# Kernel tuning notes

Measured on AMD Instinct MI355X. Metric: run time of the kernel, lower is better.

Reference implementation:

```python
import jax, jax.numpy as jnp
import numpy as np

M = 8192          # tokens (batch*seq)
K = 4096          # in_features
N = 4096          # out_features
BK = 64           # block_k (row_block of B)
BN = 64           # block_n (col_block of B)
NR = K // BK      # 64 block rows of B
NC = N // BN      # 64 block cols of B
OCC = 4           # nonzero blocks per column (and per row)
TB = NR * OCC     # total nonzero blocks = 256


def _build_indices():
    # Regular block mask: each column has OCC nonzero block-rows, each row has OCC
    # nonzero block-cols (matches BlockMask.regular invariants). Deterministic
    # construction: column c uses rows (c + s*(NR//OCC)) % NR, sorted ascending.
    step = NR // OCC
    cols = np.arange(NC)
    rows = np.sort((cols[None, :] + step * np.arange(OCC)[:, None]) % NR, axis=0)  # [OCC, NC]
    # _build_data_indices assigns data slots column-major, row-ascending within a
    # column, so column c's blocks (sorted by row) get slots c*OCC + s.
    data = cols[None, :] * OCC + np.arange(OCC)[:, None]  # [OCC, NC]
    return rows.astype(np.int32), data.astype(np.int32)


def setup_inputs() -> dict:
    key = jax.random.key(0)
    k1, k2 = jax.random.split(key)
    rows, data = _build_indices()
    return {
        "A": jax.random.normal(k1, (M, K), dtype=jnp.float32),
        "B_data": jax.random.normal(k2, (BK, BN * TB), dtype=jnp.float32) * 0.02,
        "row_indices": jnp.asarray(rows),
        "data_indices": jnp.asarray(data),
    }


def reference(A, B_data, row_indices, data_indices):
    # A: [M, K]; B_data: [BK, BN*TB]; indices: [OCC, NC]
    m, k = A.shape
    occ, nc = row_indices.shape
    bk = B_data.shape[0]
    tb = occ * nc
    bn = B_data.shape[1] // tb
    nr = k // bk
    # Gather A blocks per (sub_k, out_col): [m, occ, nc, bk]
    A_blocks = A.reshape(m, nr, bk)[:, row_indices]
    # Gather B blocks: B_data laid out as [bk, tb, bn] -> [tb, bk, bn] -> [occ, nc, bk, bn]
    B_blocks = jnp.transpose(B_data.reshape(bk, tb, bn), (1, 0, 2))[data_indices]
    # Accumulate over occ and bk (fp32 accumulation like the Triton kernel)
    C = jnp.einsum('mock,ockn->mcn', A_blocks, B_blocks,
                   preferred_element_type=jnp.float32)
    return C.reshape(m, nc * bn).astype(A.dtype)
```

## Files before the change

kernel.cpp:

```cpp
#include <hip/hip_runtime.h>
#include <hip/hip_bf16.h>

typedef __bf16 bf16x8 __attribute__((ext_vector_type(8)));
typedef float  f32x4  __attribute__((ext_vector_type(4)));

__device__ __forceinline__ void dma16(const float* g, float* l) {
    typedef const __attribute__((address_space(1))) unsigned int* gp_t;
    typedef __attribute__((address_space(3))) unsigned int*       lp_t;
    __builtin_amdgcn_global_load_lds((gp_t)(const void*)g, (lp_t)(void*)l, 16, 0, 0);
}

__global__ __launch_bounds__(256, 2) void sparse_linear_kernel(
    const float* __restrict__ A, const float* __restrict__ Bd,
    const int* __restrict__ rowi, const int* __restrict__ di,
    float* __restrict__ C)
{
    __shared__ __align__(16) float Aring[4][3][16 * 64];
    __shared__ __align__(16) unsigned short Bt[4 * 64 * 64];
    char* BtB = (char*)Bt;

    const int bid = blockIdx.x;
    const int c   = bid & 63;
    const int grp = bid >> 6;
    const int t    = threadIdx.x;
    const int lane = t & 63;
    const int w    = t >> 6;

    int rs[4], ds[4];
    #pragma unroll
    for (int s = 0; s < 4; ++s) {
        rs[s] = rowi[s * 64 + c];
        ds[s] = di[s * 64 + c];
    }
    int koff[4];
    #pragma unroll
    for (int s = 0; s < 4; ++s) koff[s] = rs[s] * 64;

    const long wrow0 = (long)grp * 1024 + w * 64;

    auto dmaA = [&](int q, int kb, int mt, int slot) {
        float* slotp = &Aring[w][slot][0];
        #pragma unroll
        for (int i = 0; i < 4; ++i) {
            const int rr  = i * 4 + (lane >> 4);
            const int kfl = (((lane & 15) * 16) ^ (rr << 4)) >> 2;
            const float* g = A + (wrow0 + q * 256 + mt * 16 + rr) * 4096 + koff[kb] + kfl;
            dma16(g, slotp + i * 256);
        }
    };

    dmaA(0, 0, 0, 0);
    dmaA(0, 0, 1, 1);
    dmaA(0, 0, 2, 2);

    {
        const int n  = t & 63;
        const int sb = t >> 6;
        const float* Bg = Bd + (long)ds[sb] * 64 + n;
        char* dst = BtB + sb * 8192 + n * 128;
        const int sw = (n & 7) << 4;
        #pragma unroll
        for (int k4 = 0; k4 < 16; ++k4) {
            union { ushort4 u4; __bf16 e[4]; } pk;
            pk.e[0] = (__bf16)Bg[(long)(4 * k4 + 0) * 16384];
            pk.e[1] = (__bf16)Bg[(long)(4 * k4 + 1) * 16384];
            pk.e[2] = (__bf16)Bg[(long)(4 * k4 + 2) * 16384];
            pk.e[3] = (__bf16)Bg[(long)(4 * k4 + 3) * 16384];
            *(ushort4*)(dst + ((8 * k4) ^ sw)) = pk.u4;
        }
    }
    __syncthreads();

    f32x4 acc[4][4];
    #pragma unroll
    for (int m = 0; m < 4; ++m)
        #pragma unroll
        for (int n2 = 0; n2 < 4; ++n2) acc[m][n2] = f32x4{0.f, 0.f, 0.f, 0.f};

    bf16x8 bfr[2][4];

    #pragma unroll 1
    for (int q = 0; q < 4; ++q) {
        const int qm3 = q % 3;

        #pragma unroll
        for (int local = 0; local < 16; ++local) {
            const int kb = local >> 2, mt = local & 3;
            int slot = qm3 + (local % 3);
            if (slot >= 3) slot -= 3;

            if (local < 3) asm volatile("s_waitcnt vmcnt(24)" ::: "memory");
            else           asm volatile("s_waitcnt vmcnt(8)"  ::: "memory");
            __builtin_amdgcn_sched_barrier(0);

            if (mt == 0) {
                const char* bbase = BtB + kb * 8192;
                #pragma unroll
                for (int kh = 0; kh < 2; ++kh)
                    #pragma unroll
                    for (int n2 = 0; n2 < 4; ++n2) {
                        const int nr = n2 * 16 + (lane & 15);
                        const int kbyte = kh * 64 + (lane >> 4) * 16;
                        bfr[kh][n2] = *(const bf16x8*)(bbase + nr * 128 + (kbyte ^ ((nr & 7) << 4)));
                    }
            }

            const char* ab = (const char*)&Aring[w][slot][0];
            const int r   = lane & 15;
            const int q32 = (lane >> 4) * 32;
            f32x4 a0 = *(const f32x4*)(ab + r * 256 + ((q32)            ^ (r << 4)));
            f32x4 a1 = *(const f32x4*)(ab + r * 256 + ((q32 + 16)       ^ (r << 4)));
            f32x4 a2 = *(const f32x4*)(ab + r * 256 + ((128 + q32)      ^ (r << 4)));
            f32x4 a3 = *(const f32x4*)(ab + r * 256 + ((128 + q32 + 16) ^ (r << 4)));
            union { bf16x8 v; __bf16 e[8]; } af0, af1;
            #pragma unroll
            for (int i = 0; i < 4; ++i) {
                af0.e[i]     = (__bf16)a0[i];
                af0.e[i + 4] = (__bf16)a1[i];
                af1.e[i]     = (__bf16)a2[i];
                af1.e[i + 4] = (__bf16)a3[i];
            }

            __builtin_amdgcn_s_setprio(1);
            #pragma unroll
            for (int kh = 0; kh < 2; ++kh) {
                const bf16x8 afv = kh ? af1.v : af0.v;
                #pragma unroll
                for (int n2 = 0; n2 < 4; ++n2)
                    acc[mt][n2] = __builtin_amdgcn_mfma_f32_16x16x32_bf16(afv, bfr[kh][n2], acc[mt][n2], 0, 0, 0);
            }
            __builtin_amdgcn_s_setprio(0);

            {
                int l2 = local + 3, q2 = q;
                if (l2 >= 16) { l2 -= 16; ++q2; }
                if (q2 > 3) q2 = 3;
                dmaA(q2, l2 >> 2, l2 & 3, slot);
            }

            if (local == 15) {
                __builtin_amdgcn_sched_barrier(0);
                #pragma unroll
                for (int mts = 0; mts < 4; ++mts) {
                    const long crow0 = wrow0 + q * 256 + mts * 16 + (lane >> 4) * 4;
                    const long col0  = (long)c * 64 + (lane & 15);
                    #pragma unroll
                    for (int n2 = 0; n2 < 4; ++n2) {
                        #pragma unroll
                        for (int v = 0; v < 4; ++v)
                            __builtin_nontemporal_store(acc[mts][n2][v],
                                &C[(crow0 + v) * 4096 + col0 + n2 * 16]);
                        acc[mts][n2] = f32x4{0.f, 0.f, 0.f, 0.f};
                    }
                }
                __builtin_amdgcn_sched_barrier(0);
            }
        }
    }

    asm volatile("s_waitcnt vmcnt(0)" ::: "memory");
}

extern "C" void kernel_launch(void* const* d_in, const int* in_sizes, int n_in,
                              void* d_out, int out_size, void* d_ws, size_t ws_size,
                              hipStream_t stream) {
    const float* A    = (const float*)d_in[0];
    const float* Bd   = (const float*)d_in[1];
    const int*   rowi = (const int*)d_in[2];
    const int*   di   = (const int*)d_in[3];
    float*       C    = (float*)d_out;

    dim3 grid(8 * 64);
    dim3 block(256);
    hipLaunchKernelGGL(sparse_linear_kernel, grid, block, 0, stream,
                       A, Bd, rowi, di, C);
}
```

Measured before the change: 56.25 us.

## Use 512-thread blocks with a 4-deep A ring and interleaved output stores

```diff
diff --git a/kernel.cpp b/kernel.cpp
--- a/kernel.cpp
+++ b/kernel.cpp
@@ -10,12 +10,12 @@
     __builtin_amdgcn_global_load_lds((gp_t)(const void*)g, (lp_t)(void*)l, 16, 0, 0);
 }
 
-__global__ __launch_bounds__(256, 2) void sparse_linear_kernel(
+__global__ __launch_bounds__(512, 2) void sparse_linear_kernel(
     const float* __restrict__ A, const float* __restrict__ Bd,
     const int* __restrict__ rowi, const int* __restrict__ di,
     float* __restrict__ C)
 {
-    __shared__ __align__(16) float Aring[4][3][16 * 64];
+    __shared__ __align__(16) float Aring[8][4][1024];
     __shared__ __align__(16) unsigned short Bt[4 * 64 * 64];
     char* BtB = (char*)Bt;
 
@@ -26,25 +26,23 @@
     const int lane = t & 63;
     const int w    = t >> 6;
 
-    int rs[4], ds[4];
+    int ds[4], koff[4];
     #pragma unroll
     for (int s = 0; s < 4; ++s) {
-        rs[s] = rowi[s * 64 + c];
-        ds[s] = di[s * 64 + c];
+        koff[s] = rowi[s * 64 + c] * 64;
+        ds[s]   = di[s * 64 + c];
     }
-    int koff[4];
-    #pragma unroll
-    for (int s = 0; s < 4; ++s) koff[s] = rs[s] * 64;
 
-    const long wrow0 = (long)grp * 1024 + w * 64;
+    const long wrow0 = (long)grp * 2048 + w * 256;
 
     auto dmaA = [&](int q, int kb, int mt, int slot) {
         float* slotp = &Aring[w][slot][0];
+        const long rbase = wrow0 + q * 64 + mt * 16;
         #pragma unroll
         for (int i = 0; i < 4; ++i) {
             const int rr  = i * 4 + (lane >> 4);
             const int kfl = (((lane & 15) * 16) ^ (rr << 4)) >> 2;
-            const float* g = A + (wrow0 + q * 256 + mt * 16 + rr) * 4096 + koff[kb] + kfl;
+            const float* g = A + (rbase + rr) * 4096 + koff[kb] + kfl;
             dma16(g, slotp + i * 256);
         }
     };
@@ -52,21 +50,23 @@
     dmaA(0, 0, 0, 0);
     dmaA(0, 0, 1, 1);
     dmaA(0, 0, 2, 2);
+    dmaA(0, 0, 3, 3);
 
     {
         const int n  = t & 63;
-        const int sb = t >> 6;
-        const float* Bg = Bd + (long)ds[sb] * 64 + n;
+        const int kh = (t >> 6) & 1;
+        const int sb = t >> 7;
+        const float* Bg = Bd + (long)ds[sb] * 64 + (long)kh * 32 * 16384 + n;
         char* dst = BtB + sb * 8192 + n * 128;
         const int sw = (n & 7) << 4;
         #pragma unroll
-        for (int k4 = 0; k4 < 16; ++k4) {
+        for (int k4 = 0; k4 < 8; ++k4) {
             union { ushort4 u4; __bf16 e[4]; } pk;
             pk.e[0] = (__bf16)Bg[(long)(4 * k4 + 0) * 16384];
             pk.e[1] = (__bf16)Bg[(long)(4 * k4 + 1) * 16384];
             pk.e[2] = (__bf16)Bg[(long)(4 * k4 + 2) * 16384];
             pk.e[3] = (__bf16)Bg[(long)(4 * k4 + 3) * 16384];
-            *(ushort4*)(dst + ((8 * k4) ^ sw)) = pk.u4;
+            *(ushort4*)(dst + ((kh * 64 + 8 * k4) ^ sw)) = pk.u4;
         }
     }
     __syncthreads();
@@ -79,19 +79,39 @@
 
     bf16x8 bfr[2][4];
 
-    #pragma unroll 1
+    #pragma unroll
     for (int q = 0; q < 4; ++q) {
-        const int qm3 = q % 3;
-
         #pragma unroll
         for (int local = 0; local < 16; ++local) {
+            const int st = q * 16 + local;
             const int kb = local >> 2, mt = local & 3;
-            int slot = qm3 + (local % 3);
-            if (slot >= 3) slot -= 3;
+            const int slot = st & 3;
 
-            if (local < 3) asm volatile("s_waitcnt vmcnt(24)" ::: "memory");
-            else           asm volatile("s_waitcnt vmcnt(8)"  ::: "memory");
-            __builtin_amdgcn_sched_barrier(0);
+            if (q == 3 && local == 13)      asm volatile("s_waitcnt vmcnt(8)"  ::: "memory");
+            else if (q == 3 && local == 14) asm volatile("s_waitcnt vmcnt(4)"  ::: "memory");
+            else if (q == 3 && local == 15) asm volatile("s_waitcnt vmcnt(0)"  ::: "memory");
+            else if (q >= 1 && (local == 1 || local == 6))
+                                            asm volatile("s_waitcnt vmcnt(28)" ::: "memory");
+            else if (q >= 1 && (local == 2 || local == 5))
+                                            asm volatile("s_waitcnt vmcnt(44)" ::: "memory");
+            else if (q >= 1 && (local == 3 || local == 4))
+                                            asm volatile("s_waitcnt vmcnt(60)" ::: "memory");
+            else                            asm volatile("s_waitcnt vmcnt(12)" ::: "memory");
+            __builtin_amdgcn_sched_barrier(0x0F);
+
+            if (q >= 1 && local < 4) {
+                const int mts = local;
+                const long crow0 = wrow0 + (q - 1) * 64 + mts * 16 + (lane >> 4) * 4;
+                const long col0  = (long)c * 64 + (lane & 15);
+                #pragma unroll
+                for (int n2 = 0; n2 < 4; ++n2) {
+                    #pragma unroll
+                    for (int v = 0; v < 4; ++v)
+                        __builtin_nontemporal_store(acc[mts][n2][v],
+                            &C[(crow0 + v) * 4096 + col0 + n2 * 16]);
+                    acc[mts][n2] = f32x4{0.f, 0.f, 0.f, 0.f};
+                }
+            }
 
             if (mt == 0) {
                 const char* bbase = BtB + kb * 8192;
@@ -121,6 +141,11 @@
                 af1.e[i + 4] = (__bf16)a3[i];
             }
 
+            if (st + 4 < 64) {
+                const int st2 = st + 4;
+                dmaA(st2 >> 4, (st2 >> 2) & 3, st2 & 3, slot);
+            }
+
             __builtin_amdgcn_s_setprio(1);
             #pragma unroll
             for (int kh = 0; kh < 2; ++kh) {
@@ -130,35 +155,21 @@
                     acc[mt][n2] = __builtin_amdgcn_mfma_f32_16x16x32_bf16(afv, bfr[kh][n2], acc[mt][n2], 0, 0, 0);
             }
             __builtin_amdgcn_s_setprio(0);
-
-            {
-                int l2 = local + 3, q2 = q;
-                if (l2 >= 16) { l2 -= 16; ++q2; }
-                if (q2 > 3) q2 = 3;
-                dmaA(q2, l2 >> 2, l2 & 3, slot);
-            }
-
-            if (local == 15) {
-                __builtin_amdgcn_sched_barrier(0);
-                #pragma unroll
-                for (int mts = 0; mts < 4; ++mts) {
-                    const long crow0 = wrow0 + q * 256 + mts * 16 + (lane >> 4) * 4;
-                    const long col0  = (long)c * 64 + (lane & 15);
-                    #pragma unroll
-                    for (int n2 = 0; n2 < 4; ++n2) {
-                        #pragma unroll
-                        for (int v = 0; v < 4; ++v)
-                            __builtin_nontemporal_store(acc[mts][n2][v],
-                                &C[(crow0 + v) * 4096 + col0 + n2 * 16]);
-                        acc[mts][n2] = f32x4{0.f, 0.f, 0.f, 0.f};
-                    }
-                }
-                __builtin_amdgcn_sched_barrier(0);
-            }
         }
     }
 
     asm volatile("s_waitcnt vmcnt(0)" ::: "memory");
+    #pragma unroll
+    for (int mts = 0; mts < 4; ++mts) {
+        const long crow0 = wrow0 + 3 * 64 + mts * 16 + (lane >> 4) * 4;
+        const long col0  = (long)c * 64 + (lane & 15);
+        #pragma unroll
+        for (int n2 = 0; n2 < 4; ++n2)
+            #pragma unroll
+            for (int v = 0; v < 4; ++v)
+                __builtin_nontemporal_store(acc[mts][n2][v],
+                    &C[(crow0 + v) * 4096 + col0 + n2 * 16]);
+    }
 }
 
 extern "C" void kernel_launch(void* const* d_in, const int* in_sizes, int n_in,
@@ -170,8 +181,8 @@
     const int*   di   = (const int*)d_in[3];
     float*       C    = (float*)d_out;
 
-    dim3 grid(8 * 64);
-    dim3 block(256);
+    dim3 grid(4 * 64);
+    dim3 block(512);
     hipLaunchKernelGGL(sparse_linear_kernel, grid, block, 0, stream,
                        A, Bd, rowi, di, C);
 }
```

After: 83.49 us. 1.48x slower.

## Pre-convert B to bf16 in workspace and double the grid with smaller row tiles

Applied to the files above, without the earlier changes.

```diff
diff --git a/kernel.cpp b/kernel.cpp
--- a/kernel.cpp
+++ b/kernel.cpp
@@ -10,14 +10,30 @@
     __builtin_amdgcn_global_load_lds((gp_t)(const void*)g, (lp_t)(void*)l, 16, 0, 0);
 }
 
-__global__ __launch_bounds__(256, 2) void sparse_linear_kernel(
-    const float* __restrict__ A, const float* __restrict__ Bd,
+__global__ __launch_bounds__(256) void transpose_B_kernel(
+    const float* __restrict__ Bd, unsigned short* __restrict__ ws)
+{
+    const int d  = blockIdx.x;
+    const int t  = threadIdx.x;
+    const int n  = t >> 2;
+    const int kq = t & 3;
+    const float* src = Bd + (long)d * 64 + n;
+    unsigned short* dst = ws + (long)d * 4096 + n * 64 + kq * 16;
+    union { ushort4 u4[4]; __bf16 e[16]; } pk;
+    #pragma unroll
+    for (int j = 0; j < 16; ++j)
+        pk.e[j] = (__bf16)src[(long)(kq * 16 + j) * 16384];
+    #pragma unroll
+    for (int i = 0; i < 4; ++i)
+        *(ushort4*)(dst + i * 4) = pk.u4[i];
+}
+
+__global__ __launch_bounds__(256, 3) void sparse_linear_kernel(
+    const float* __restrict__ A, const unsigned short* __restrict__ wsB,
     const int* __restrict__ rowi, const int* __restrict__ di,
     float* __restrict__ C)
 {
     __shared__ __align__(16) float Aring[4][3][16 * 64];
-    __shared__ __align__(16) unsigned short Bt[4 * 64 * 64];
-    char* BtB = (char*)Bt;
 
     const int bid = blockIdx.x;
     const int c   = bid & 63;
@@ -26,25 +42,24 @@
     const int lane = t & 63;
     const int w    = t >> 6;
 
-    int rs[4], ds[4];
+    int koff[4];
+    long boff[4];
     #pragma unroll
     for (int s = 0; s < 4; ++s) {
-        rs[s] = rowi[s * 64 + c];
-        ds[s] = di[s * 64 + c];
+        koff[s] = rowi[s * 64 + c] * 64;
+        boff[s] = (long)di[s * 64 + c] * 4096;
     }
-    int koff[4];
-    #pragma unroll
-    for (int s = 0; s < 4; ++s) koff[s] = rs[s] * 64;
 
-    const long wrow0 = (long)grp * 1024 + w * 64;
+    const long wrow0 = (long)grp * 512 + w * 128;
 
     auto dmaA = [&](int q, int kb, int mt, int slot) {
         float* slotp = &Aring[w][slot][0];
+        const long rbase = wrow0 + q * 64 + mt * 16;
         #pragma unroll
         for (int i = 0; i < 4; ++i) {
             const int rr  = i * 4 + (lane >> 4);
             const int kfl = (((lane & 15) * 16) ^ (rr << 4)) >> 2;
-            const float* g = A + (wrow0 + q * 256 + mt * 16 + rr) * 4096 + koff[kb] + kfl;
+            const float* g = A + (rbase + rr) * 4096 + koff[kb] + kfl;
             dma16(g, slotp + i * 256);
         }
     };
@@ -52,24 +67,6 @@
     dmaA(0, 0, 0, 0);
     dmaA(0, 0, 1, 1);
     dmaA(0, 0, 2, 2);
-
-    {
-        const int n  = t & 63;
-        const int sb = t >> 6;
-        const float* Bg = Bd + (long)ds[sb] * 64 + n;
-        char* dst = BtB + sb * 8192 + n * 128;
-        const int sw = (n & 7) << 4;
-        #pragma unroll
-        for (int k4 = 0; k4 < 16; ++k4) {
-            union { ushort4 u4; __bf16 e[4]; } pk;
-            pk.e[0] = (__bf16)Bg[(long)(4 * k4 + 0) * 16384];
-            pk.e[1] = (__bf16)Bg[(long)(4 * k4 + 1) * 16384];
-            pk.e[2] = (__bf16)Bg[(long)(4 * k4 + 2) * 16384];
-            pk.e[3] = (__bf16)Bg[(long)(4 * k4 + 3) * 16384];
-            *(ushort4*)(dst + ((8 * k4) ^ sw)) = pk.u4;
-        }
-    }
-    __syncthreads();
 
     f32x4 acc[4][4];
     #pragma unroll
@@ -80,28 +77,33 @@
     bf16x8 bfr[2][4];
 
     #pragma unroll 1
-    for (int q = 0; q < 4; ++q) {
-        const int qm3 = q % 3;
-
+    for (int q = 0; q < 2; ++q) {
         #pragma unroll
         for (int local = 0; local < 16; ++local) {
+            const int st = q * 16 + local;
             const int kb = local >> 2, mt = local & 3;
-            int slot = qm3 + (local % 3);
+            int slot = q + (local % 3);
             if (slot >= 3) slot -= 3;
 
-            if (local < 3) asm volatile("s_waitcnt vmcnt(24)" ::: "memory");
-            else           asm volatile("s_waitcnt vmcnt(8)"  ::: "memory");
+            if (local < 3) {
+                if (q == 0) asm volatile("s_waitcnt vmcnt(8)"  ::: "memory");
+                else        asm volatile("s_waitcnt vmcnt(24)" ::: "memory");
+            } else if ((local & 3) == 1 || (local & 3) == 2) {
+                asm volatile("s_waitcnt vmcnt(12)" ::: "memory");
+            } else {
+                asm volatile("s_waitcnt vmcnt(8)" ::: "memory");
+            }
             __builtin_amdgcn_sched_barrier(0);
 
             if (mt == 0) {
-                const char* bbase = BtB + kb * 8192;
+                const unsigned short* bsrc = wsB + boff[kb];
                 #pragma unroll
                 for (int kh = 0; kh < 2; ++kh)
                     #pragma unroll
                     for (int n2 = 0; n2 < 4; ++n2) {
                         const int nr = n2 * 16 + (lane & 15);
-                        const int kbyte = kh * 64 + (lane >> 4) * 16;
-                        bfr[kh][n2] = *(const bf16x8*)(bbase + nr * 128 + (kbyte ^ ((nr & 7) << 4)));
+                        const int k0 = kh * 32 + (lane >> 4) * 8;
+                        bfr[kh][n2] = *(const bf16x8*)(bsrc + nr * 64 + k0);
                     }
             }
 
@@ -121,6 +123,13 @@
                 af1.e[i + 4] = (__bf16)a3[i];
             }
 
+            {
+                int l2 = local + 3, q2 = q;
+                if (l2 >= 16) { l2 -= 16; ++q2; }
+                if (q2 > 1) { q2 = 1; l2 = 15; }
+                dmaA(q2, l2 >> 2, l2 & 3, slot);
+            }
+
             __builtin_amdgcn_s_setprio(1);
             #pragma unroll
             for (int kh = 0; kh < 2; ++kh) {
@@ -131,18 +140,11 @@
             }
             __builtin_amdgcn_s_setprio(0);
 
-            {
-                int l2 = local + 3, q2 = q;
-                if (l2 >= 16) { l2 -= 16; ++q2; }
-                if (q2 > 3) q2 = 3;
-                dmaA(q2, l2 >> 2, l2 & 3, slot);
-            }
-
             if (local == 15) {
                 __builtin_amdgcn_sched_barrier(0);
                 #pragma unroll
                 for (int mts = 0; mts < 4; ++mts) {
-                    const long crow0 = wrow0 + q * 256 + mts * 16 + (lane >> 4) * 4;
+                    const long crow0 = wrow0 + q * 64 + mts * 16 + (lane >> 4) * 4;
                     const long col0  = (long)c * 64 + (lane & 15);
                     #pragma unroll
                     for (int n2 = 0; n2 < 4; ++n2) {
@@ -169,9 +171,12 @@
     const int*   rowi = (const int*)d_in[2];
     const int*   di   = (const int*)d_in[3];
     float*       C    = (float*)d_out;
+    unsigned short* ws = (unsigned short*)d_ws;
 
-    dim3 grid(8 * 64);
+    hipLaunchKernelGGL(transpose_B_kernel, dim3(256), dim3(256), 0, stream, Bd, ws);
+
+    dim3 grid(16 * 64);
     dim3 block(256);
     hipLaunchKernelGGL(sparse_linear_kernel, grid, block, 0, stream,
-                       A, Bd, rowi, di, C);
+                       A, ws, rowi, di, C);
 }
```

New measurement: 125.7 us. +123.5%, slower.
